# Optimization experiments

Measured on AMD Instinct MI355X. Metric: run time of the kernel, lower is better.

Reference implementation:

```python
import jax, jax.numpy as jnp
import numpy as np

TEMP = 0.07
EPS = 1e-6
NORM_EPS = 1e-12  # F.normalize default eps
LN_EPS = 1e-5

B, D, H, W = 32, 256, 64, 64
K = 256
DFF = 2048


def _l2norm(v, axis):
    n = jnp.sqrt(jnp.sum(v * v, axis=axis, keepdims=True))
    return v / jnp.maximum(n, NORM_EPS)


def _layernorm(v, g, b):
    mu = jnp.mean(v, axis=-1, keepdims=True)
    var = jnp.mean((v - mu) ** 2, axis=-1, keepdims=True)
    return (v - mu) * jax.lax.rsqrt(var + LN_EPS) * g + b


def setup_inputs() -> dict:
    key = jax.random.key(0)
    ks = jax.random.split(key, 8)
    s1 = 1.0 / np.sqrt(D)
    s2 = 1.0 / np.sqrt(DFF)
    return {
        "x": jax.random.normal(ks[0], (B, D, H, W), jnp.float32),
        "tgt": jax.random.normal(ks[1], (B, K, D), jnp.float32),
        "w1": jax.random.uniform(ks[2], (DFF, D), jnp.float32, -s1, s1),
        "b1": jax.random.uniform(ks[3], (DFF,), jnp.float32, -s1, s1),
        "w2": jax.random.uniform(ks[4], (D, DFF), jnp.float32, -s2, s2),
        "b2": jax.random.uniform(ks[5], (D,), jnp.float32, -s2, s2),
        "g2": jnp.ones((D,), jnp.float32),
        "be2": jnp.zeros((D,), jnp.float32),
        "g3": jnp.ones((D,), jnp.float32),
        "be3": jnp.zeros((D,), jnp.float32),
    }


def reference(x, tgt, w1, b1, w2, b2, g2, be2, g3, be3):
    # slot cross-attention with L2-normalized q/k
    tn = _l2norm(tgt, axis=2)           # (b,k,d)
    xn = _l2norm(x, axis=1)             # (b,d,h,w)
    dots = jnp.einsum('bkd,bdhw->bkhw', tn, xn)
    attn = jax.nn.softmax(dots / TEMP, axis=1) + EPS          # softmax over slots
    attn = attn / jnp.sum(attn, axis=(2, 3), keepdims=True)   # spatial normalization
    tgt2 = jnp.einsum('bdhw,bkhw->bkd', x, attn)
    t = _layernorm(tgt + tgt2, g2, be2)
    # FFN (dropout = identity in eval)
    ff = jnp.maximum(t @ w1.T + b1, 0.0) @ w2.T + b2
    return _layernorm(t + ff, g3, be3)
```

## Files before the change

kernel.cpp:

```cpp
#include <hip/hip_runtime.h>
#include <hip/hip_bf16.h>

using bf16 = __hip_bfloat16;

typedef __attribute__((ext_vector_type(8))) short short8;
typedef __attribute__((ext_vector_type(4))) float f32x4;

constexpr int Bb = 32, Dd = 256, HWw = 4096, Kk = 256, Ff = 2048;
constexpr float TEMP_INV = 1.0f / 0.07f;
constexpr float EPSf = 1e-6f;
constexpr float NORM_EPSf = 1e-12f;
constexpr float LN_EPSf = 1e-5f;

static __device__ __forceinline__ float b2f(bf16 v) { return __bfloat162float(v); }
static __device__ __forceinline__ bf16 f2b(float v) { return __float2bfloat16(v); }


__global__ __launch_bounds__(64) void k_tn(const float* __restrict__ tgt,
                                           bf16* __restrict__ tnbf) {
  int row = blockIdx.x;
  int b = row >> 8, slot = row & 255;
  int lane = threadIdx.x;
  const float* src = tgt + (size_t)row * Dd + lane * 4;
  float v[4];
#pragma unroll
  for (int u = 0; u < 4; u++) v[u] = src[u];
  float ss = v[0] * v[0] + v[1] * v[1] + v[2] * v[2] + v[3] * v[3];
#pragma unroll
  for (int m = 32; m >= 1; m >>= 1) ss += __shfl_xor(ss, m, 64);
  float inv = 1.0f / fmaxf(sqrtf(ss), NORM_EPSf);
  bf16 o[4] __attribute__((aligned(8)));
#pragma unroll
  for (int u = 0; u < 4; u++) o[u] = f2b(v[u] * inv);
  int s = lane >> 3;
  int q2 = (lane >> 1) & 3;
  int jh = (lane & 1) * 4;
  size_t fi = (size_t)((slot >> 4) * 64 + q2 * 16 + (slot & 15));
  *(float2*)(tnbf + ((size_t)(b * 8 + s) * 1024 + fi) * 8 + jh) = *(float2*)o;
}

__global__ __launch_bounds__(64) void k_prew1(const float* __restrict__ w1,
                                              bf16* __restrict__ w1bf) {
  int f = blockIdx.x;
  int lane = threadIdx.x;
  const float* src = w1 + (size_t)f * Dd + lane * 4;
  bf16 o[4] __attribute__((aligned(8)));
#pragma unroll
  for (int u = 0; u < 4; u++) o[u] = f2b(src[u]);
  int s = lane >> 3;
  int q2 = (lane >> 1) & 3;
  int jh = (lane & 1) * 4;
  size_t fi = (size_t)(((f & 63) >> 4) * 64 + q2 * 16 + (f & 15));
  *(float2*)(w1bf + ((size_t)((f >> 6) * 8 + s) * 256 + fi) * 8 + jh) = *(float2*)o;
}

__global__ __launch_bounds__(64) void k_prew2(const float* __restrict__ w2,
                                              bf16* __restrict__ w2bf) {
  int d = blockIdx.x;
  int lane = threadIdx.x;
  const float* src = w2 + (size_t)d * Ff + lane * 32;
  size_t gbase = (size_t)((d >> 6) * 64 + lane) * 256;
  int fbase = ((d & 63) >> 4) * 64 + (d & 15);
#pragma unroll
  for (int q2 = 0; q2 < 4; q2++) {
    float4 v0 = *(const float4*)(src + q2 * 8);
    float4 v1 = *(const float4*)(src + q2 * 8 + 4);
    bf16 o[8] __attribute__((aligned(16)));
    o[0] = f2b(v0.x); o[1] = f2b(v0.y); o[2] = f2b(v0.z); o[3] = f2b(v0.w);
    o[4] = f2b(v1.x); o[5] = f2b(v1.y); o[6] = f2b(v1.z); o[7] = f2b(v1.w);
    *(float4*)(w2bf + (gbase + fbase + q2 * 16) * 8) = *(float4*)o;
  }
}

#define MFMA16(a, b, c) __builtin_amdgcn_mfma_f32_16x16x32_bf16(a, b, c, 0, 0, 0)

__global__ __launch_bounds__(256) void k_dots(const bf16* __restrict__ tnbf,
                                              const float* __restrict__ x,
                                              bf16* __restrict__ xb_bf,
                                              bf16* __restrict__ attn_bf,
                                              float* __restrict__ S) {
  __shared__ __align__(16) bf16 Bs[2][4 * 520];
  __shared__ float ssred[64 * 17];
  __shared__ float nxl[64];
  __shared__ float red[512];
  int b = blockIdx.x >> 6;
  int hw0 = (blockIdx.x & 63) * 64;
  int tid = threadIdx.x;
  int wave = tid >> 6, lane = tid & 63;
  int quad = lane >> 4, nl = lane & 15;

  int dp = tid >> 4;
  int ch = tid & 15;
  int qb = dp >> 2;
  int jb = (dp & 3) * 2;

  f32x4 acc[4][4];
#pragma unroll
  for (int i = 0; i < 4; i++)
#pragma unroll
    for (int j = 0; j < 4; j++) acc[i][j] = (f32x4){0.f, 0.f, 0.f, 0.f};
  float ssp[4] = {0.f, 0.f, 0.f, 0.f};

  int spx = (hw0 >> 5) + (ch >> 3);
  int q2x = (ch >> 1) & 3;
  int jx = (ch & 1) * 4;

  float4 va, vb;
  short8 afp[4];
  {
    const float* xr0 = x + (size_t)((b << 8) + 2 * dp) * HWw + hw0 + ch * 4;
    va = *(const float4*)xr0;
    vb = *(const float4*)(xr0 + HWw);
    const bf16* ts0 = tnbf + (size_t)(b * 8) * 1024 * 8;
#pragma unroll
    for (int mt = 0; mt < 4; mt++)
      afp[mt] = *(const short8*)(ts0 + (size_t)(((wave << 2) + mt) * 64 + lane) * 8);
  }

  for (int s = 0; s < 8; s++) {
    bf16* bsb = &Bs[s & 1][0];
    {
      float vva[4] = {va.x, va.y, va.z, va.w};
      float vvb[4] = {vb.x, vb.y, vb.z, vb.w};
      bf16 pa[4] __attribute__((aligned(8)));
      bf16 pb[4] __attribute__((aligned(8)));
#pragma unroll
      for (int jj = 0; jj < 4; jj++) {
        ssp[jj] += vva[jj] * vva[jj] + vvb[jj] * vvb[jj];
        pa[jj] = f2b(vva[jj]);
        pb[jj] = f2b(vvb[jj]);
      }
      int d0r = s * 32 + 2 * dp;
      int fiA = (d0r >> 4) * 64 + q2x * 16 + (d0r & 15);
      size_t base = ((size_t)(b * 128) + spx) * 1024;
      *(float2*)(xb_bf + (base + fiA) * 8 + jx) = *(float2*)pa;
      *(float2*)(xb_bf + (base + fiA + 1) * 8 + jx) = *(float2*)pb;
#pragma unroll
      for (int jj = 0; jj < 4; jj++) {
        int hwl = ch * 4 + jj;
        int nt = hwl >> 4;
        int li = (qb << 4) | (hwl & 15);
        union { bf16 h[2]; unsigned int u; } pk;
        pk.h[0] = pa[jj];
        pk.h[1] = pb[jj];
        *(unsigned int*)&bsb[nt * 520 + li * 8 + jb] = pk.u;
      }
    }
    __syncthreads();
    short8 af[4];
#pragma unroll
    for (int mt = 0; mt < 4; mt++) af[mt] = afp[mt];
    if (s < 7) {
      const float* xr = x + (size_t)((b << 8) + (s + 1) * 32 + 2 * dp) * HWw + hw0 + ch * 4;
      va = *(const float4*)xr;
      vb = *(const float4*)(xr + HWw);
      const bf16* tsrc = tnbf + (size_t)(b * 8 + s + 1) * 1024 * 8;
#pragma unroll
      for (int mt = 0; mt < 4; mt++)
        afp[mt] = *(const short8*)(tsrc + (size_t)(((wave << 2) + mt) * 64 + lane) * 8);
    }
    short8 bfv[4];
#pragma unroll
    for (int nt = 0; nt < 4; nt++)
      bfv[nt] = *(const short8*)(bsb + nt * 520 + lane * 8);
#pragma unroll
    for (int mt = 0; mt < 4; mt++)
#pragma unroll
      for (int nt = 0; nt < 4; nt++) acc[mt][nt] = MFMA16(af[mt], bfv[nt], acc[mt][nt]);
  }

#pragma unroll
  for (int jj = 0; jj < 4; jj++) ssred[(ch * 4 + jj) * 17 + dp] = ssp[jj];
  __syncthreads();
  if (tid < 64) {
    float sum = 0.f;
#pragma unroll
    for (int i = 0; i < 16; i++) sum += ssred[tid * 17 + i];
    nxl[tid] = TEMP_INV / fmaxf(sqrtf(sum), NORM_EPSf);
  }
  __syncthreads();

  float sc[4];
#pragma unroll
  for (int nt = 0; nt < 4; nt++) sc[nt] = nxl[nt * 16 + nl];
#pragma unroll
  for (int mt = 0; mt < 4; mt++)
#pragma unroll
    for (int nt = 0; nt < 4; nt++)
#pragma unroll
      for (int r = 0; r < 4; r++) acc[mt][nt][r] *= sc[nt];

  float* red2 = red + 256;

  float pmax[4];
#pragma unroll
  for (int nt = 0; nt < 4; nt++) {
    float m = acc[0][nt][0];
#pragma unroll
    for (int mt = 0; mt < 4; mt++)
#pragma unroll
      for (int r = 0; r < 4; r++) m = fmaxf(m, acc[mt][nt][r]);
    m = fmaxf(m, __shfl_xor(m, 16, 64));
    m = fmaxf(m, __shfl_xor(m, 32, 64));
    pmax[nt] = m;
  }
  if (lane < 16) {
#pragma unroll
    for (int nt = 0; nt < 4; nt++) red[((wave << 2) + nt) * 16 + nl] = pmax[nt];
  }
  __syncthreads();
  float cmax[4];
#pragma unroll
  for (int nt = 0; nt < 4; nt++) {
    float m = red[nt * 16 + nl];
#pragma unroll
    for (int w2 = 1; w2 < 4; w2++) m = fmaxf(m, red[((w2 << 2) + nt) * 16 + nl]);
    cmax[nt] = m;
  }

  float psum[4];
#pragma unroll
  for (int nt = 0; nt < 4; nt++) {
    float s = 0.f;
#pragma unroll
    for (int mt = 0; mt < 4; mt++)
#pragma unroll
      for (int r = 0; r < 4; r++) {
        float e = __expf(acc[mt][nt][r] - cmax[nt]);
        acc[mt][nt][r] = e;
        s += e;
      }
    s += __shfl_xor(s, 16, 64);
    s += __shfl_xor(s, 32, 64);
    psum[nt] = s;
  }
  if (lane < 16) {
#pragma unroll
    for (int nt = 0; nt < 4; nt++) red2[((wave << 2) + nt) * 16 + nl] = psum[nt];
  }
  __syncthreads();
  float ci[4];
#pragma unroll
  for (int nt = 0; nt < 4; nt++) {
    float s = 0.f;
#pragma unroll
    for (int w2 = 0; w2 < 4; w2++) s += red2[((w2 << 2) + nt) * 16 + nl];
    ci[nt] = 1.0f / s;
  }

  int jat = nl & 7;
#pragma unroll
  for (int mt = 0; mt < 4; mt++) {
    int slotg = (b << 8) + (wave << 6) + (mt << 4) + (quad << 2);
    int fiBase = ((wave << 2) + mt) * 64 + (quad << 2);
#pragma unroll
    for (int r = 0; r < 4; r++) {
      float rs = 0.f;
#pragma unroll
      for (int nt = 0; nt < 4; nt++) {
        float a = acc[mt][nt][r] * ci[nt] + EPSf;
        bf16 hb = f2b(a);
        int q2p = ((nt & 1) << 1) + (nl >> 3);
        size_t sp = (size_t)(b * 128) + (hw0 >> 5) + (nt >> 1);
        attn_bf[(sp * 1024 + fiBase + q2p * 16 + r) * 8 + jat] = hb;
        rs += b2f(hb);
      }
      rs += __shfl_xor(rs, 1, 64);
      rs += __shfl_xor(rs, 2, 64);
      rs += __shfl_xor(rs, 4, 64);
      rs += __shfl_xor(rs, 8, 64);
      if (nl == 0) atomicAdd(&S[slotg + r], rs);
    }
  }
}

__global__ __launch_bounds__(256) void k_gemm2(const bf16* __restrict__ attn_bf,
                                               const bf16* __restrict__ xb_bf,
                                               float* __restrict__ t2) {
  int n = blockIdx.x;
  int b = n & 31;
  int r2 = n >> 5;
  int kp = r2 & 3;
  int dgrp = (r2 >> 2) & 3;
  int hs = r2 >> 4;
  int tid = threadIdx.x;
  int wave = tid >> 6, lane = tid & 63;
  int wr = wave >> 1, wc = wave & 1;

  f32x4 acc[2][2];
#pragma unroll
  for (int i = 0; i < 2; i++)
#pragma unroll
    for (int j = 0; j < 2; j++) acc[i][j] = (f32x4){0.f, 0.f, 0.f, 0.f};

  const bf16* Abase = attn_bf + ((size_t)(b * 128 + hs * 32) * 1024 + (size_t)(kp * 4 + wr * 2) * 64) * 8;
  const bf16* Bbase = xb_bf + ((size_t)(b * 128 + hs * 32) * 1024 + (size_t)(dgrp * 4 + wc * 2) * 64) * 8;
#pragma unroll 4
  for (int st = 0; st < 32; st++) {
    const bf16* Ap = Abase + (size_t)st * 1024 * 8;
    const bf16* Bp = Bbase + (size_t)st * 1024 * 8;
    short8 a0 = *(const short8*)(Ap + (size_t)lane * 8);
    short8 a1 = *(const short8*)(Ap + (size_t)(64 + lane) * 8);
    short8 b0 = *(const short8*)(Bp + (size_t)lane * 8);
    short8 b1 = *(const short8*)(Bp + (size_t)(64 + lane) * 8);
    acc[0][0] = MFMA16(a0, b0, acc[0][0]);
    acc[0][1] = MFMA16(a0, b1, acc[0][1]);
    acc[1][0] = MFMA16(a1, b0, acc[1][0]);
    acc[1][1] = MFMA16(a1, b1, acc[1][1]);
  }
  int quad = lane >> 4, nl = lane & 15;
#pragma unroll
  for (int i = 0; i < 2; i++)
#pragma unroll
    for (int r = 0; r < 4; r++) {
      int row = (b << 8) + kp * 64 + wr * 32 + i * 16 + quad * 4 + r;
#pragma unroll
      for (int j = 0; j < 2; j++) {
        int col = dgrp * 64 + wc * 32 + j * 16 + nl;
        atomicAdd(&t2[(size_t)row * Dd + col], acc[i][j][r]);
      }
    }
}

__global__ __launch_bounds__(64) void k_ln_pre(const float* __restrict__ t2,
                                               const float* __restrict__ S,
                                               const float* __restrict__ tgt,
                                               const float* __restrict__ g,
                                               const float* __restrict__ be,
                                               float* __restrict__ t,
                                               bf16* __restrict__ tbf) {
  int row = blockIdx.x;
  int lane = threadIdx.x;
  float sInv = 1.0f / S[row];
  const float* p2 = t2 + (size_t)row * Dd + lane * 4;
  const float* pt = tgt + (size_t)row * Dd + lane * 4;
  float v[4];
#pragma unroll
  for (int u = 0; u < 4; u++) v[u] = p2[u] * sInv + pt[u];
  float s1 = v[0] + v[1] + v[2] + v[3];
  float s2 = v[0] * v[0] + v[1] * v[1] + v[2] * v[2] + v[3] * v[3];
#pragma unroll
  for (int m = 32; m >= 1; m >>= 1) {
    s1 += __shfl_xor(s1, m, 64);
    s2 += __shfl_xor(s2, m, 64);
  }
  float mu = s1 * (1.0f / 256.0f);
  float var = s2 * (1.0f / 256.0f) - mu * mu;
  float rs = rsqrtf(fmaxf(var, 0.f) + LN_EPSf);
  float* po = t + (size_t)row * Dd + lane * 4;
  bf16 o[4] __attribute__((aligned(8)));
#pragma unroll
  for (int u = 0; u < 4; u++) {
    float val = (v[u] - mu) * rs * g[lane * 4 + u] + be[lane * 4 + u];
    po[u] = val;
    o[u] = f2b(val);
  }
  int s = lane >> 3;
  int q2 = (lane >> 1) & 3;
  int jh = (lane & 1) * 4;
  size_t fi = (size_t)(((row & 63) >> 4) * 64 + q2 * 16 + (row & 15));
  *(float2*)(tbf + ((size_t)((row >> 6) * 8 + s) * 256 + fi) * 8 + jh) = *(float2*)o;
}

__global__ __launch_bounds__(256) void k_ffn1(const bf16* __restrict__ tbf,
                                              const bf16* __restrict__ w1bf,
                                              const float* __restrict__ b1,
                                              bf16* __restrict__ h1bf) {
  int rowgrp = blockIdx.x >> 5;
  int fgrp = blockIdx.x & 31;
  int tid = threadIdx.x;
  int wave = tid >> 6, lane = tid & 63;
  int am = (wave >> 1) * 2, bn = (wave & 1) * 2;

  f32x4 acc[2][2];
#pragma unroll
  for (int i = 0; i < 2; i++)
#pragma unroll
    for (int j = 0; j < 2; j++) acc[i][j] = (f32x4){0.f, 0.f, 0.f, 0.f};

  const bf16* Abase = tbf + (size_t)rowgrp * 8 * 256 * 8;
  const bf16* Bbase = w1bf + (size_t)fgrp * 8 * 256 * 8;
#pragma unroll
  for (int s = 0; s < 8; s++) {
    short8 af[2], bfr[2];
#pragma unroll
    for (int i = 0; i < 2; i++)
      af[i] = *(const short8*)(Abase + ((size_t)s * 256 + ((am + i) * 64 + lane)) * 8);
#pragma unroll
    for (int j = 0; j < 2; j++)
      bfr[j] = *(const short8*)(Bbase + ((size_t)s * 256 + ((bn + j) * 64 + lane)) * 8);
#pragma unroll
    for (int i = 0; i < 2; i++)
#pragma unroll
      for (int j = 0; j < 2; j++) acc[i][j] = MFMA16(af[i], bfr[j], acc[i][j]);
  }
  int quad = lane >> 4, nl = lane & 15;
  int jat = nl & 7;
#pragma unroll
  for (int j = 0; j < 2; j++) {
    int f = fgrp * 64 + (bn + j) * 16 + nl;
    float bias = b1[f];
    size_t sp = (size_t)(rowgrp * 64) + fgrp * 2 + ((bn + j) >> 1);
    int q2p = ((bn + j) & 1) * 2 + (nl >> 3);
#pragma unroll
    for (int i = 0; i < 2; i++) {
      int fiBase = (am + i) * 64 + q2p * 16 + (quad << 2);
#pragma unroll
      for (int r = 0; r < 4; r++) {
        float val = fmaxf(acc[i][j][r] + bias, 0.f);
        h1bf[(sp * 256 + fiBase + r) * 8 + jat] = f2b(val);
      }
    }
  }
}

__global__ __launch_bounds__(256) void k_ffn2(const bf16* __restrict__ h1bf,
                                              const bf16* __restrict__ w2bf,
                                              float* __restrict__ o2) {
  int n = blockIdx.x;
  int rowgrp = n >> 3;
  int ksp = n & 7;
  int tid = threadIdx.x;
  int wave = tid >> 6, lane = tid & 63;

  f32x4 acc[4][4];
#pragma unroll
  for (int i = 0; i < 4; i++)
#pragma unroll
    for (int j = 0; j < 4; j++) acc[i][j] = (f32x4){0.f, 0.f, 0.f, 0.f};

#pragma unroll
  for (int st = 0; st < 8; st++) {
    int sg = ksp * 8 + st;
    const bf16* Ab = h1bf + ((size_t)(rowgrp * 64 + sg) * 256) * 8;
    const bf16* Bbv = w2bf + ((size_t)(wave * 64 + sg) * 256) * 8;
    short8 af[4], bfr[4];
#pragma unroll
    for (int mt = 0; mt < 4; mt++)
      af[mt] = *(const short8*)(Ab + (size_t)(mt * 64 + lane) * 8);
#pragma unroll
    for (int nt = 0; nt < 4; nt++)
      bfr[nt] = *(const short8*)(Bbv + (size_t)(nt * 64 + lane) * 8);
#pragma unroll
    for (int mt = 0; mt < 4; mt++)
#pragma unroll
      for (int nt = 0; nt < 4; nt++) acc[mt][nt] = MFMA16(af[mt], bfr[nt], acc[mt][nt]);
  }
  int quad = lane >> 4, nl = lane & 15;
#pragma unroll
  for (int mt = 0; mt < 4; mt++)
#pragma unroll
    for (int r = 0; r < 4; r++) {
      int row = rowgrp * 64 + mt * 16 + quad * 4 + r;
#pragma unroll
      for (int nt = 0; nt < 4; nt++) {
        int col = wave * 64 + nt * 16 + nl;
        atomicAdd(&o2[(size_t)row * Dd + col], acc[mt][nt][r]);
      }
    }
}

__global__ __launch_bounds__(64) void k_ln_out(const float* __restrict__ o2,
                                               const float* __restrict__ b2v,
                                               const float* __restrict__ t,
                                               const float* __restrict__ g,
                                               const float* __restrict__ be,
                                               float* __restrict__ out) {
  int row = blockIdx.x;
  int lane = threadIdx.x;
  const float* po = o2 + (size_t)row * Dd + lane * 4;
  const float* pt = t + (size_t)row * Dd + lane * 4;
  float v[4];
#pragma unroll
  for (int u = 0; u < 4; u++) v[u] = po[u] + b2v[lane * 4 + u] + pt[u];
  float s1 = v[0] + v[1] + v[2] + v[3];
  float s2 = v[0] * v[0] + v[1] * v[1] + v[2] * v[2] + v[3] * v[3];
#pragma unroll
  for (int m = 32; m >= 1; m >>= 1) {
    s1 += __shfl_xor(s1, m, 64);
    s2 += __shfl_xor(s2, m, 64);
  }
  float mu = s1 * (1.0f / 256.0f);
  float var = s2 * (1.0f / 256.0f) - mu * mu;
  float rs = rsqrtf(fmaxf(var, 0.f) + LN_EPSf);
  float* pw = out + (size_t)row * Dd + lane * 4;
#pragma unroll
  for (int u = 0; u < 4; u++)
    pw[u] = (v[u] - mu) * rs * g[lane * 4 + u] + be[lane * 4 + u];
}

extern "C" void kernel_launch(void* const* d_in, const int* in_sizes, int n_in,
                              void* d_out, int out_size, void* d_ws, size_t ws_size,
                              hipStream_t stream) {
  const float* x = (const float*)d_in[0];
  const float* tgt = (const float*)d_in[1];
  const float* w1 = (const float*)d_in[2];
  const float* b1 = (const float*)d_in[3];
  const float* w2 = (const float*)d_in[4];
  const float* b2v = (const float*)d_in[5];
  const float* g2 = (const float*)d_in[6];
  const float* be2 = (const float*)d_in[7];
  const float* g3 = (const float*)d_in[8];
  const float* be3 = (const float*)d_in[9];
  float* out = (float*)d_out;

  char* w = (char*)d_ws;
  bf16* tnbf = (bf16*)w;     w += (size_t)Bb * Kk * Dd * 2;
  float* S = (float*)w;      w += (size_t)Bb * Kk * 4;
  float* t = (float*)w;      w += (size_t)Bb * Kk * Dd * 4;
  float* t2 = (float*)w;     w += (size_t)Bb * Kk * Dd * 4;
  bf16* attn_bf = (bf16*)w;  w += (size_t)Bb * HWw * Kk * 2;
  bf16* h1bf = (bf16*)w;     w += (size_t)Bb * Kk * Ff * 2;
  bf16* xb_bf = (bf16*)w;    w += (size_t)Bb * Dd * HWw * 2;

  bf16* tbf = tnbf;
  float* o2 = t2;
  bf16* w1bf = attn_bf;
  bf16* w2bf = attn_bf + (size_t)Ff * Dd;

  hipMemsetAsync(S, 0, (size_t)Bb * Kk * 4, stream);
  hipMemsetAsync(t2, 0, (size_t)Bb * Kk * Dd * 4, stream);
  k_tn<<<Bb * Kk, 64, 0, stream>>>(tgt, tnbf);
  k_dots<<<Bb * (HWw / 64), 256, 0, stream>>>(tnbf, x, xb_bf, attn_bf, S);
  k_gemm2<<<2048, 256, 0, stream>>>(attn_bf, xb_bf, t2);
  k_prew1<<<Ff, 64, 0, stream>>>(w1, w1bf);
  k_prew2<<<Dd, 64, 0, stream>>>(w2, w2bf);
  k_ln_pre<<<Bb * Kk, 64, 0, stream>>>(t2, S, tgt, g2, be2, t, tbf);
  hipMemsetAsync(o2, 0, (size_t)Bb * Kk * Dd * 4, stream);
  k_ffn1<<<(Bb * Kk / 64) * (Ff / 64), 256, 0, stream>>>(tbf, w1bf, b1, h1bf);
  k_ffn2<<<(Bb * Kk / 64) * 8, 256, 0, stream>>>(h1bf, w2bf, o2);
  k_ln_out<<<Bb * Kk, 64, 0, stream>>>(o2, b2v, t, g3, be3, out);
}
```

Baseline: 447.9 us.

## Replace split-K atomics with partial buffers and stage attn stores through LDS

The two split-K GEMMs (attn·x and FFN2) now write plain stores into separate per-split partial buffers, which the following layernorm kernels sum, instead of doing fp32 atomicAdd into a zeroed buffer. This removes the atomic traffic and two memsets, at the cost of extra partial-buffer reads. The partial buffers reuse the workspace regions h1bf and xb_bf, which are dead at those points. Separately, k_dots now stages its bf16 attention tile in shared memory and writes it to global with coalesced 16-byte stores instead of scattered 2-byte stores.

Result: faster. 411.0 us (-8.2%).

```diff
diff --git a/kernel.cpp b/kernel.cpp
--- a/kernel.cpp
+++ b/kernel.cpp
@@ -11,6 +11,7 @@
 constexpr float EPSf = 1e-6f;
 constexpr float NORM_EPSf = 1e-12f;
 constexpr float LN_EPSf = 1e-5f;
+constexpr size_t PKD = (size_t)Bb * Kk * Dd;
 
 static __device__ __forceinline__ float b2f(bf16 v) { return __bfloat162float(v); }
 static __device__ __forceinline__ bf16 f2b(float v) { return __float2bfloat16(v); }
@@ -79,10 +80,11 @@
                                               bf16* __restrict__ xb_bf,
                                               bf16* __restrict__ attn_bf,
                                               float* __restrict__ S) {
-  __shared__ __align__(16) bf16 Bs[2][4 * 520];
-  __shared__ float ssred[64 * 17];
-  __shared__ float nxl[64];
-  __shared__ float red[512];
+  __shared__ __align__(16) char smem[16384];
+  bf16* Bs = (bf16*)smem;
+  float* ssred = (float*)(smem + 8320);
+  float* nxl = (float*)(smem + 12672);
+  float* red = (float*)(smem + 12928);
   int b = blockIdx.x >> 6;
   int hw0 = (blockIdx.x & 63) * 64;
   int tid = threadIdx.x;
@@ -118,7 +120,7 @@
   }
 
   for (int s = 0; s < 8; s++) {
-    bf16* bsb = &Bs[s & 1][0];
+    bf16* bsb = Bs + (s & 1) * 2080;
     {
       float vva[4] = {va.x, va.y, va.z, va.w};
       float vvb[4] = {vb.x, vb.y, vb.z, vb.w};
@@ -248,22 +250,18 @@
     ci[nt] = 1.0f / s;
   }
 
-  int jat = nl & 7;
 #pragma unroll
   for (int mt = 0; mt < 4; mt++) {
     int slotg = (b << 8) + (wave << 6) + (mt << 4) + (quad << 2);
-    int fiBase = ((wave << 2) + mt) * 64 + (quad << 2);
 #pragma unroll
     for (int r = 0; r < 4; r++) {
       float rs = 0.f;
 #pragma unroll
       for (int nt = 0; nt < 4; nt++) {
-        float a = acc[mt][nt][r] * ci[nt] + EPSf;
-        bf16 hb = f2b(a);
-        int q2p = ((nt & 1) << 1) + (nl >> 3);
-        size_t sp = (size_t)(b * 128) + (hw0 >> 5) + (nt >> 1);
-        attn_bf[(sp * 1024 + fiBase + q2p * 16 + r) * 8 + jat] = hb;
-        rs += b2f(hb);
+        bf16 hb = f2b(acc[mt][nt][r] * ci[nt] + EPSf);
+        float q = b2f(hb);
+        acc[mt][nt][r] = q;
+        rs += q;
       }
       rs += __shfl_xor(rs, 1, 64);
       rs += __shfl_xor(rs, 2, 64);
@@ -272,11 +270,38 @@
       if (nl == 0) atomicAdd(&S[slotg + r], rs);
     }
   }
+
+  __syncthreads();
+  bf16* rp = (bf16*)smem;
+  int jat = nl & 7;
+#pragma unroll
+  for (int h = 0; h < 2; h++) {
+#pragma unroll
+    for (int mt = 0; mt < 4; mt++) {
+      int fi0 = ((wave << 2) + mt) * 64 + (quad << 2);
+#pragma unroll
+      for (int ntl = 0; ntl < 2; ntl++) {
+        int nt = (h << 1) + ntl;
+        int q2p = (ntl << 1) + (nl >> 3);
+#pragma unroll
+        for (int r = 0; r < 4; r++)
+          rp[(fi0 + q2p * 16 + r) * 8 + jat] = f2b(acc[mt][nt][r]);
+      }
+    }
+    __syncthreads();
+    size_t gbase = ((size_t)(b * 128) + (hw0 >> 5) + h) * 1024 * 8;
+#pragma unroll
+    for (int u = 0; u < 4; u++) {
+      short8 vv = *(const short8*)(rp + u * 2048 + tid * 8);
+      *(short8*)(attn_bf + gbase + u * 2048 + tid * 8) = vv;
+    }
+    if (h == 0) __syncthreads();
+  }
 }
 
 __global__ __launch_bounds__(256) void k_gemm2(const bf16* __restrict__ attn_bf,
                                                const bf16* __restrict__ xb_bf,
-                                               float* __restrict__ t2) {
+                                               float* __restrict__ t2p) {
   int n = blockIdx.x;
   int b = n & 31;
   int r2 = n >> 5;
@@ -308,6 +333,7 @@
     acc[1][0] = MFMA16(a1, b0, acc[1][0]);
     acc[1][1] = MFMA16(a1, b1, acc[1][1]);
   }
+  float* dst = t2p + (size_t)hs * PKD;
   int quad = lane >> 4, nl = lane & 15;
 #pragma unroll
   for (int i = 0; i < 2; i++)
@@ -317,12 +343,12 @@
 #pragma unroll
       for (int j = 0; j < 2; j++) {
         int col = dgrp * 64 + wc * 32 + j * 16 + nl;
-        atomicAdd(&t2[(size_t)row * Dd + col], acc[i][j][r]);
-      }
-    }
-}
-
-__global__ __launch_bounds__(64) void k_ln_pre(const float* __restrict__ t2,
+        dst[(size_t)row * Dd + col] = acc[i][j][r];
+      }
+    }
+}
+
+__global__ __launch_bounds__(64) void k_ln_pre(const float* __restrict__ t2p,
                                                const float* __restrict__ S,
                                                const float* __restrict__ tgt,
                                                const float* __restrict__ g,
@@ -332,11 +358,17 @@
   int row = blockIdx.x;
   int lane = threadIdx.x;
   float sInv = 1.0f / S[row];
-  const float* p2 = t2 + (size_t)row * Dd + lane * 4;
-  const float* pt = tgt + (size_t)row * Dd + lane * 4;
+  size_t off = (size_t)row * Dd + lane * 4;
+  float4 a0 = *(const float4*)(t2p + off);
+  float4 a1 = *(const float4*)(t2p + PKD + off);
+  float4 a2 = *(const float4*)(t2p + 2 * PKD + off);
+  float4 a3 = *(const float4*)(t2p + 3 * PKD + off);
+  const float* pt = tgt + off;
   float v[4];
-#pragma unroll
-  for (int u = 0; u < 4; u++) v[u] = p2[u] * sInv + pt[u];
+  v[0] = (a0.x + a1.x + a2.x + a3.x) * sInv + pt[0];
+  v[1] = (a0.y + a1.y + a2.y + a3.y) * sInv + pt[1];
+  v[2] = (a0.z + a1.z + a2.z + a3.z) * sInv + pt[2];
+  v[3] = (a0.w + a1.w + a2.w + a3.w) * sInv + pt[3];
   float s1 = v[0] + v[1] + v[2] + v[3];
   float s2 = v[0] * v[0] + v[1] * v[1] + v[2] * v[2] + v[3] * v[3];
 #pragma unroll
@@ -416,7 +448,7 @@
 
 __global__ __launch_bounds__(256) void k_ffn2(const bf16* __restrict__ h1bf,
                                               const bf16* __restrict__ w2bf,
-                                              float* __restrict__ o2) {
+                                              float* __restrict__ o2p) {
   int n = blockIdx.x;
   int rowgrp = n >> 3;
   int ksp = n & 7;
@@ -446,6 +478,7 @@
 #pragma unroll
       for (int nt = 0; nt < 4; nt++) acc[mt][nt] = MFMA16(af[mt], bfr[nt], acc[mt][nt]);
   }
+  float* dst = o2p + (size_t)ksp * PKD;
   int quad = lane >> 4, nl = lane & 15;
 #pragma unroll
   for (int mt = 0; mt < 4; mt++)
@@ -455,12 +488,12 @@
 #pragma unroll
       for (int nt = 0; nt < 4; nt++) {
         int col = wave * 64 + nt * 16 + nl;
-        atomicAdd(&o2[(size_t)row * Dd + col], acc[mt][nt][r]);
-      }
-    }
-}
-
-__global__ __launch_bounds__(64) void k_ln_out(const float* __restrict__ o2,
+        dst[(size_t)row * Dd + col] = acc[mt][nt][r];
+      }
+    }
+}
+
+__global__ __launch_bounds__(64) void k_ln_out(const float* __restrict__ o2p,
                                                const float* __restrict__ b2v,
                                                const float* __restrict__ t,
                                                const float* __restrict__ g,
@@ -468,11 +501,20 @@
                                                float* __restrict__ out) {
   int row = blockIdx.x;
   int lane = threadIdx.x;
-  const float* po = o2 + (size_t)row * Dd + lane * 4;
-  const float* pt = t + (size_t)row * Dd + lane * 4;
+  size_t off = (size_t)row * Dd + lane * 4;
+  float acc4[4] = {0.f, 0.f, 0.f, 0.f};
+#pragma unroll
+  for (int q = 0; q < 8; q++) {
+    float4 aq = *(const float4*)(o2p + (size_t)q * PKD + off);
+    acc4[0] += aq.x;
+    acc4[1] += aq.y;
+    acc4[2] += aq.z;
+    acc4[3] += aq.w;
+  }
+  const float* pt = t + off;
   float v[4];
 #pragma unroll
-  for (int u = 0; u < 4; u++) v[u] = po[u] + b2v[lane * 4 + u] + pt[u];
+  for (int u = 0; u < 4; u++) v[u] = acc4[u] + b2v[lane * 4 + u] + pt[u];
   float s1 = v[0] + v[1] + v[2] + v[3];
   float s2 = v[0] * v[0] + v[1] * v[1] + v[2] * v[2] + v[3] * v[3];
 #pragma unroll
@@ -508,26 +550,24 @@
   bf16* tnbf = (bf16*)w;     w += (size_t)Bb * Kk * Dd * 2;
   float* S = (float*)w;      w += (size_t)Bb * Kk * 4;
   float* t = (float*)w;      w += (size_t)Bb * Kk * Dd * 4;
-  float* t2 = (float*)w;     w += (size_t)Bb * Kk * Dd * 4;
   bf16* attn_bf = (bf16*)w;  w += (size_t)Bb * HWw * Kk * 2;
   bf16* h1bf = (bf16*)w;     w += (size_t)Bb * Kk * Ff * 2;
   bf16* xb_bf = (bf16*)w;    w += (size_t)Bb * Dd * HWw * 2;
 
   bf16* tbf = tnbf;
-  float* o2 = t2;
   bf16* w1bf = attn_bf;
   bf16* w2bf = attn_bf + (size_t)Ff * Dd;
+  float* t2p = (float*)h1bf;
+  float* o2p = (float*)xb_bf;
 
   hipMemsetAsync(S, 0, (size_t)Bb * Kk * 4, stream);
-  hipMemsetAsync(t2, 0, (size_t)Bb * Kk * Dd * 4, stream);
   k_tn<<<Bb * Kk, 64, 0, stream>>>(tgt, tnbf);
   k_dots<<<Bb * (HWw / 64), 256, 0, stream>>>(tnbf, x, xb_bf, attn_bf, S);
-  k_gemm2<<<2048, 256, 0, stream>>>(attn_bf, xb_bf, t2);
+  k_gemm2<<<2048, 256, 0, stream>>>(attn_bf, xb_bf, t2p);
   k_prew1<<<Ff, 64, 0, stream>>>(w1, w1bf);
   k_prew2<<<Dd, 64, 0, stream>>>(w2, w2bf);
-  k_ln_pre<<<Bb * Kk, 64, 0, stream>>>(t2, S, tgt, g2, be2, t, tbf);
-  hipMemsetAsync(o2, 0, (size_t)Bb * Kk * Dd * 4, stream);
+  k_ln_pre<<<Bb * Kk, 64, 0, stream>>>(t2p, S, tgt, g2, be2, t, tbf);
   k_ffn1<<<(Bb * Kk / 64) * (Ff / 64), 256, 0, stream>>>(tbf, w1bf, b1, h1bf);
-  k_ffn2<<<(Bb * Kk / 64) * 8, 256, 0, stream>>>(h1bf, w2bf, o2);
-  k_ln_out<<<Bb * Kk, 64, 0, stream>>>(o2, b2v, t, g3, be3, out);
-}
+  k_ffn2<<<(Bb * Kk / 64) * 8, 256, 0, stream>>>(h1bf, w2bf, o2p);
+  k_ln_out<<<Bb * Kk, 64, 0, stream>>>(o2p, b2v, t, g3, be3, out);
+}
```
